# Performance work log

Measured on AMD Instinct MI355X. Metric: run time of the kernel, lower is better.

The kernel has to match this reference:

```python
import jax, jax.numpy as jnp
import numpy as np

B, L, V, E, H, C, OUT = 128, 256, 50000, 300, 128, 4, 2
D = 2 * H  # features_size == sequence_max_len (required by the conv kernel width)
FS = (2, 3, 4, 5)


def _p(key, shape, s=0.05):
    return (jax.random.normal(key, shape) * s).astype(jnp.float32)


def setup_inputs() -> dict:
    key = jax.random.key(0)
    ks = jax.random.split(key, 32)
    emb = _p(ks[0], (V, E)).at[0].set(0.0)  # padding_idx=0
    inp = {
        'utterance': jax.random.randint(ks[1], (B, L), 1, V, dtype=jnp.int32),
        'seq_lengths': jnp.full((B,), L, dtype=jnp.int32),
        'emb': emb,
        'w_ih0': _p(ks[2], (2, 3 * H, E)), 'w_hh0': _p(ks[3], (2, 3 * H, H)),
        'b_ih0': _p(ks[4], (2, 3 * H)), 'b_hh0': _p(ks[5], (2, 3 * H)),
        'w_ih1': _p(ks[6], (2, 3 * H, 2 * H)), 'w_hh1': _p(ks[7], (2, 3 * H, H)),
        'b_ih1': _p(ks[8], (2, 3 * H)), 'b_hh1': _p(ks[9], (2, 3 * H)),
        'att_w': _p(ks[10], (C, D, D)), 'att_b': _p(ks[11], (C,)),
        'att_wv2': _p(ks[12], (C, D, D)), 'att_bv': _p(ks[13], (C, D)),
        'att_wv1': _p(ks[14], (C, D)),
        'fc_w': _p(ks[15], (OUT, sum(FS))), 'fc_b': _p(ks[16], (OUT,)),
    }
    for i, fs in enumerate(FS):
        inp[f'conv_w{i}'] = _p(ks[17 + 2 * i], (fs, C, fs, L))
        inp[f'conv_b{i}'] = _p(ks[18 + 2 * i], (fs,))
    return inp


def _gru_dir(x, w_ih, w_hh, b_ih, b_hh, reverse):
    # x: (B,T,in) -> (B,T,H); PyTorch GRU cell equations, eval mode (no dropout)
    gx = jnp.einsum('bti,gi->btg', x, w_ih) + b_ih  # (B,T,3H)

    def step(h, gxt):
        gh = h @ w_hh.T + b_hh
        xr, xz, xn = jnp.split(gxt, 3, axis=-1)
        hr, hz, hn = jnp.split(gh, 3, axis=-1)
        r = jax.nn.sigmoid(xr + hr)
        z = jax.nn.sigmoid(xz + hz)
        n = jnp.tanh(xn + r * hn)
        h = (1.0 - z) * n + z * h
        return h, h

    h0 = jnp.zeros((x.shape[0], w_hh.shape[1]), x.dtype)
    _, ys = jax.lax.scan(step, h0, jnp.swapaxes(gx, 0, 1), reverse=reverse)
    return jnp.swapaxes(ys, 0, 1)


def _bigru_layer(x, w_ih, w_hh, b_ih, b_hh):
    f = _gru_dir(x, w_ih[0], w_hh[0], b_ih[0], b_hh[0], False)
    b = _gru_dir(x, w_ih[1], w_hh[1], b_ih[1], b_hh[1], True)
    return jnp.concatenate([f, b], axis=-1)


def _forward(utterance, emb, w_ih0, w_hh0, b_ih0, b_hh0, w_ih1, w_hh1, b_ih1, b_hh1,
             att_w, att_b, att_wv2, att_bv, att_wv1, conv_params, fc_w, fc_b):
    x = emb[utterance]                                   # (B,L,E)
    x = _bigru_layer(x, w_ih0, w_hh0, b_ih0, b_hh0)      # (B,L,2H)
    x = _bigru_layer(x, w_ih1, w_hh1, b_ih1, b_hh1)      # (B,L,D)
    # --- AMCNN attention, vectorized over channels c ---
    mat = jnp.einsum('bld,cde->cble', x, att_w)          # mat_l per channel (C,B,L,D)
    # M_l[b,i,j] = <inputs[b,i], mat_l[b,j]> + b_l  (the torch tile/sum written as matmul)
    M = jnp.einsum('bid,cbjd->cbij', x, mat) + att_b[:, None, None, None]
    a = jax.nn.softmax(jnp.tanh(M).sum(axis=3), axis=2)  # scalar attention (C,B,L)
    g = jax.nn.sigmoid(jnp.einsum('bld,cde->cble', x, att_wv2) + att_bv[:, None, None, :])
    aa = jax.nn.softmax(jnp.einsum('cble,ce->cbl', g, att_wv1), axis=2)  # vector attn (C,B,L)
    new = jnp.einsum('cbl,bld->cbd', aa, x)              # weighted sum, broadcast over L
    Cf = a[..., None] * x[None] + new[:, :, None, :]     # (C,B,L,D)
    Cf = jnp.transpose(Cf, (1, 0, 2, 3))                 # (B,C,L,D)
    # --- conv blocks: Conv2d(k=(fs,L)) + ReLU + MaxPool((L-fs+1,1)) + Flatten ---
    pools = []
    for w, bi in conv_params:
        y = jax.lax.conv_general_dilated(Cf, w, (1, 1), 'VALID',
                                         dimension_numbers=('NCHW', 'OIHW', 'NCHW'))
        y = jax.nn.relu(y + bi[None, :, None, None])     # (B,fs,L-fs+1,1)
        pools.append(y.max(axis=(2, 3)))                 # (B,fs)
    feats = jnp.concatenate(pools, axis=-1)              # (B,sum(FS))
    return feats @ fc_w.T + fc_b                         # (B,OUT)


def reference(utterance, seq_lengths, emb, w_ih0, w_hh0, b_ih0, b_hh0,
              w_ih1, w_hh1, b_ih1, b_hh1, att_w, att_b, att_wv2, att_bv, att_wv1,
              conv_w0, conv_b0, conv_w1, conv_b1, conv_w2, conv_b2, conv_w3, conv_b3,
              fc_w, fc_b):
    # seq_lengths are all == L, so pack/pad_packed is an identity here
    conv_params = ((conv_w0, conv_b0), (conv_w1, conv_b1), (conv_w2, conv_b2), (conv_w3, conv_b3))
    return _forward(utterance, emb, w_ih0, w_hh0, b_ih0, b_hh0, w_ih1, w_hh1, b_ih1, b_hh1,
                    att_w, att_b, att_wv2, att_bv, att_wv1, conv_params, fc_w, fc_b)
```

## Files before the change

kernel.cpp:

```cpp
#include <hip/hip_runtime.h>
#include <hip/hip_bf16.h>
#include <hip/hip_fp16.h>

#define Bn  128
#define Ln  256
#define En  300
#define Hn  128
#define Cn  4
#define Dn  256
#define G3n 384
#define BLn (Bn * Ln)

typedef __hip_bfloat16 bf16;
typedef short s16x8 __attribute__((ext_vector_type(8)));
typedef float f32x4 __attribute__((ext_vector_type(4)));
typedef _Float16 h16x2 __attribute__((ext_vector_type(2)));

__device__ __forceinline__ float ldf(const float* p) { return *p; }
__device__ __forceinline__ float ldf(const bf16* p)  { return __bfloat162float(*p); }
__device__ __forceinline__ void stf(float* p, float v) { *p = v; }
__device__ __forceinline__ void stf(bf16* p, float v)  { *p = __float2bfloat16(v); }

__device__ __forceinline__ ushort f2bf(float f) {
    bf16 h = __float2bfloat16(f);
    return *reinterpret_cast<ushort*>(&h);
}

#if __has_builtin(__builtin_amdgcn_fdot2)
__device__ __forceinline__ float dot2f(h16x2 w, h16x2 h, float c) {
    return __builtin_amdgcn_fdot2(w, h, c, false);
}
#else
__device__ __forceinline__ float dot2f(h16x2 w, h16x2 h, float c) {
    return fmaf((float)w[0], (float)h[0], fmaf((float)w[1], (float)h[1], c));
}
#endif
#define BCH(x) __builtin_bit_cast(h16x2, x)

template<class OT, bool GATHER, int SM>
__global__ __launch_bounds__(256)
void gemm_mfma(const float* __restrict__ A, const float* __restrict__ W,
               const float* __restrict__ bias, OT* __restrict__ Cout,
               const int* __restrict__ gidx, int M, int N, int K)
{
    __shared__ ushort Asm[128 * 40];
    __shared__ ushort Bsm[128 * 40];
    const int bm = blockIdx.y * 128, bn = blockIdx.x * 128;
    const int tid = threadIdx.x;
    const int lane = tid & 63, w = tid >> 6, wr = w >> 1, wc = w & 1;

    const float* arow[4];
    const float* brow[4];
#pragma unroll
    for (int u = 0; u < 4; ++u) {
        const int idx = tid + u * 256;
        const int m = idx >> 3;
        arow[u] = A + (size_t)(GATHER ? gidx[bm + m] : (bm + m)) * K;
        brow[u] = W + (size_t)(bn + m) * K;
    }

    f32x4 acc[4][4] = {};
    const int nkt = (K + 31) >> 5;
    for (int kt = 0; kt < nkt; ++kt) {
        const int k0 = kt << 5;
#pragma unroll
        for (int u = 0; u < 4; ++u) {
            const int idx = tid + u * 256;
            const int m = idx >> 3, kq = idx & 7;
            const int kb = k0 + kq * 4;
            float4 v, q;
            if (kb + 4 <= K) {
                v = *(const float4*)(arow[u] + kb);
                q = *(const float4*)(brow[u] + kb);
            } else {
                v.x = kb + 0 < K ? arow[u][kb + 0] : 0.f;
                v.y = kb + 1 < K ? arow[u][kb + 1] : 0.f;
                v.z = kb + 2 < K ? arow[u][kb + 2] : 0.f;
                v.w = kb + 3 < K ? arow[u][kb + 3] : 0.f;
                q.x = kb + 0 < K ? brow[u][kb + 0] : 0.f;
                q.y = kb + 1 < K ? brow[u][kb + 1] : 0.f;
                q.z = kb + 2 < K ? brow[u][kb + 2] : 0.f;
                q.w = kb + 3 < K ? brow[u][kb + 3] : 0.f;
            }
            *(ushort4*)&Asm[m * 40 + kq * 4] =
                make_ushort4(f2bf(v.x), f2bf(v.y), f2bf(v.z), f2bf(v.w));
            *(ushort4*)&Bsm[m * 40 + kq * 4] =
                make_ushort4(f2bf(q.x), f2bf(q.y), f2bf(q.z), f2bf(q.w));
        }
        __syncthreads();
        s16x8 af[4], bfr[4];
#pragma unroll
        for (int t = 0; t < 4; ++t) {
            af[t]  = *(const s16x8*)&Asm[(wr * 64 + t * 16 + (lane & 15)) * 40 + (lane >> 4) * 8];
            bfr[t] = *(const s16x8*)&Bsm[(wc * 64 + t * 16 + (lane & 15)) * 40 + (lane >> 4) * 8];
        }
#pragma unroll
        for (int mf = 0; mf < 4; ++mf)
#pragma unroll
            for (int nf = 0; nf < 4; ++nf)
                acc[mf][nf] = __builtin_amdgcn_mfma_f32_16x16x32_bf16(
                    af[mf], bfr[nf], acc[mf][nf], 0, 0, 0);
        __syncthreads();
    }

#pragma unroll
    for (int mf = 0; mf < 4; ++mf)
#pragma unroll
        for (int nf = 0; nf < 4; ++nf) {
            const int col = bn + wc * 64 + nf * 16 + (lane & 15);
            const float bv_ = bias ? bias[col] : 0.f;
#pragma unroll
            for (int i = 0; i < 4; ++i) {
                const int row = bm + wr * 64 + mf * 16 + (lane >> 4) * 4 + i;
                const float v = acc[mf][nf][i] + bv_;
                if (SM == 1)
                    stf(&Cout[((size_t)(row >> 8) * N + col) * 256 + (row & 255)], v);
                else
                    stf(&Cout[(size_t)row * N + col], v);
            }
        }
}

__global__ __launch_bounds__(384, 1)
void gru_scan_b128(const bf16* __restrict__ gx, const float* __restrict__ w_hh,
                   const float* __restrict__ b_hh, float* __restrict__ out)
{
    const int b = blockIdx.x, dir = blockIdx.y;
    const int r = threadIdx.x;
    __shared__ __align__(16) ushort wl[384 * 136];
    __shared__ __align__(16) h16x2 hp[64];
    __shared__ float h_sh[128];
    __shared__ float rs[128], zs[128], gxn[128], ghn[128];

    const float* wbase = w_hh + (size_t)dir * G3n * Hn;
    for (int idx = r; idx < G3n * 64; idx += 384) {
        const int row = idx >> 6, k2 = idx & 63;
        const float2 v = *(const float2*)(wbase + row * Hn + 2 * k2);
        h16x2 p; p[0] = (_Float16)v.x; p[1] = (_Float16)v.y;
        *(h16x2*)&wl[row * 136 + 2 * k2] = p;
    }
    if (r < 64) { h16x2 z; z[0] = (_Float16)0.f; z[1] = (_Float16)0.f; hp[r] = z; }
    if (r < 128) h_sh[r] = 0.f;
    const float bh = b_hh[dir * G3n + r];
    __syncthreads();

    const size_t g0 = (size_t)b * Ln * 768 + dir * G3n + r
                      + (dir ? (size_t)(Ln - 1) * 768 : 0);
    const long gstep = dir ? -768L : 768L;
    float gcur = ldf(&gx[g0]);
    float gnx  = ldf(&gx[g0 + gstep]);

    const ushort* wrow = &wl[r * 136];

    for (int s = 0; s < Ln; ++s) {
        const int t = dir ? (Ln - 1 - s) : s;
        float gn2 = 0.f;
        if (s + 2 < Ln) gn2 = ldf(&gx[g0 + (long)(s + 2) * gstep]);

        float a0 = 0.f, a1 = 0.f, a2 = 0.f, a3 = 0.f;
#pragma unroll
        for (int j = 0; j < 16; ++j) {
            const float4 wv = *(const float4*)&wrow[8 * j];
            const float4 hv = *(const float4*)&hp[4 * j];
            a0 = dot2f(BCH(wv.x), BCH(hv.x), a0);
            a1 = dot2f(BCH(wv.y), BCH(hv.y), a1);
            a2 = dot2f(BCH(wv.z), BCH(hv.z), a2);
            a3 = dot2f(BCH(wv.w), BCH(hv.w), a3);
        }
        const float acc = (a0 + a1) + (a2 + a3) + bh;

        if (r < 128)      rs[r]       = 1.f / (1.f + expf(-(gcur + acc)));
        else if (r < 256) zs[r - 128] = 1.f / (1.f + expf(-(gcur + acc)));
        else { gxn[r - 256] = gcur; ghn[r - 256] = acc; }
        __syncthreads();

        if (r < 64) {
            const int j0 = 2 * r, j1 = j0 + 1;
            const float nn0 = tanhf(gxn[j0] + rs[j0] * ghn[j0]);
            const float nn1 = tanhf(gxn[j1] + rs[j1] * ghn[j1]);
            const float h0 = (1.f - zs[j0]) * nn0 + zs[j0] * h_sh[j0];
            const float h1 = (1.f - zs[j1]) * nn1 + zs[j1] * h_sh[j1];
            h_sh[j0] = h0; h_sh[j1] = h1;
            h16x2 pr; pr[0] = (_Float16)h0; pr[1] = (_Float16)h1;
            hp[r] = pr;
            *(float2*)&out[((size_t)b * Ln + t) * Dn + dir * Hn + j0] =
                make_float2(h0, h1);
        }
        __syncthreads();
        gcur = gnx; gnx = gn2;
    }
}

__global__ __launch_bounds__(256)
void attn_score_mfma(const float* __restrict__ x, const float* __restrict__ matc,
                     const float* __restrict__ attb, int c, float* __restrict__ sout)
{
    const int it = blockIdx.x, b = blockIdx.y;
    const float* A  = x    + ((size_t)b * 256 + it * 128) * 256;
    const float* Bm = matc + (size_t)b * 65536;
    __shared__ ushort Xs[128 * 40];
    __shared__ ushort Ms[128 * 40];
    const int tid = threadIdx.x, lane = tid & 63, w = tid >> 6;
    const float bc = attb[c];
    float psum[2][4] = {};

    for (int jt = 0; jt < 2; ++jt) {
        f32x4 acc[2][8] = {};
        for (int kt = 0; kt < 8; ++kt) {
            const int k0 = kt << 5;
#pragma unroll
            for (int u = 0; u < 4; ++u) {
                const int idx = tid + u * 256;
                const int m = idx >> 3, kq = idx & 7;
                const float4 v = *(const float4*)(A + (size_t)m * 256 + k0 + kq * 4);
                const float4 q = *(const float4*)(Bm + (size_t)(jt * 128 + m) * 256 + k0 + kq * 4);
                *(ushort4*)&Xs[m * 40 + kq * 4] =
                    make_ushort4(f2bf(v.x), f2bf(v.y), f2bf(v.z), f2bf(v.w));
                *(ushort4*)&Ms[m * 40 + kq * 4] =
                    make_ushort4(f2bf(q.x), f2bf(q.y), f2bf(q.z), f2bf(q.w));
            }
            __syncthreads();
            s16x8 af[2], bfr[8];
#pragma unroll
            for (int t = 0; t < 2; ++t)
                af[t] = *(const s16x8*)&Xs[(w * 32 + t * 16 + (lane & 15)) * 40 + (lane >> 4) * 8];
#pragma unroll
            for (int t = 0; t < 8; ++t)
                bfr[t] = *(const s16x8*)&Ms[(t * 16 + (lane & 15)) * 40 + (lane >> 4) * 8];
#pragma unroll
            for (int mf = 0; mf < 2; ++mf)
#pragma unroll
                for (int nf = 0; nf < 8; ++nf)
                    acc[mf][nf] = __builtin_amdgcn_mfma_f32_16x16x32_bf16(
                        af[mf], bfr[nf], acc[mf][nf], 0, 0, 0);
            __syncthreads();
        }
#pragma unroll
        for (int mf = 0; mf < 2; ++mf)
#pragma unroll
            for (int nf = 0; nf < 8; ++nf)
#pragma unroll
                for (int i = 0; i < 4; ++i)
                    psum[mf][i] += tanhf(acc[mf][nf][i] + bc);
    }

#pragma unroll
    for (int mf = 0; mf < 2; ++mf)
#pragma unroll
        for (int i = 0; i < 4; ++i) {
            float v = psum[mf][i];
            v += __shfl_xor(v, 1); v += __shfl_xor(v, 2);
            v += __shfl_xor(v, 4); v += __shfl_xor(v, 8);
            if ((lane & 15) == 0)
                sout[b * 256 + it * 128 + w * 32 + mf * 16 + (lane >> 4) * 4 + i] = v;
        }
}

__global__ __launch_bounds__(256)
void gv_reduce(const float* __restrict__ gv, const float* __restrict__ bv,
               const float* __restrict__ wv1, float* __restrict__ al)
{
    const int row = blockIdx.x * 4 + (threadIdx.x >> 6);
    const int l = threadIdx.x & 63;
    const float4 v  = *(const float4*)(gv + (size_t)row * 256 + l * 4);
    const float4 bb = *(const float4*)(bv + l * 4);
    const float4 w  = *(const float4*)(wv1 + l * 4);
    float s = w.x / (1.f + expf(-(v.x + bb.x)))
            + w.y / (1.f + expf(-(v.y + bb.y)))
            + w.z / (1.f + expf(-(v.z + bb.z)))
            + w.w / (1.f + expf(-(v.w + bb.w)));
#pragma unroll
    for (int m = 1; m < 64; m <<= 1) s += __shfl_xor(s, m);
    if (l == 0) al[row] = s;
}

__global__ void transpose256(const float* __restrict__ src, float* __restrict__ dst)
{
    const float* s = src + (size_t)blockIdx.x * 65536;
    float* d = dst + (size_t)blockIdx.x * 65536;
    __shared__ float t[32][33];
    const int tx = threadIdx.x & 31, ty8 = threadIdx.x >> 5;
    for (int bi = 0; bi < 8; ++bi)
        for (int bj = 0; bj < 8; ++bj) {
            __syncthreads();
            for (int r = ty8; r < 32; r += 8)
                t[r][tx] = s[(size_t)(bi * 32 + r) * 256 + bj * 32 + tx];
            __syncthreads();
            for (int r = ty8; r < 32; r += 8)
                d[(size_t)(bj * 32 + r) * 256 + bi * 32 + tx] = t[tx][r];
        }
}

__global__ void softmax256(const float* __restrict__ in, float* __restrict__ out)
{
    __shared__ float red[256];
    const int row = blockIdx.x, t = threadIdx.x;
    const float v = in[(size_t)row * 256 + t];
    red[t] = v; __syncthreads();
    for (int off = 128; off; off >>= 1) {
        if (t < off) red[t] = fmaxf(red[t], red[t + off]);
        __syncthreads();
    }
    const float mx = red[0]; __syncthreads();
    const float e = expf(v - mx);
    red[t] = e; __syncthreads();
    for (int off = 128; off; off >>= 1) {
        if (t < off) red[t] += red[t + off];
        __syncthreads();
    }
    out[(size_t)row * 256 + t] = e / red[0];
}

__global__ void weighted_sum_kernel(const float* __restrict__ aa,
                                    const float* __restrict__ x,
                                    float* __restrict__ outnew)
{
    const int b = blockIdx.x, c = blockIdx.y, d = threadIdx.x;
    __shared__ float w[Ln];
    w[d] = aa[((size_t)c * Bn + b) * Ln + d];
    __syncthreads();
    float acc = 0.f;
    for (int l = 0; l < Ln; ++l)
        acc += w[l] * x[((size_t)b * Ln + l) * Dn + d];
    outnew[((size_t)c * Bn + b) * Dn + d] = acc;
}

__global__ void wpack_fill(const float* __restrict__ w0, const float* __restrict__ w1,
                           const float* __restrict__ w2, const float* __restrict__ w3,
                           float* __restrict__ wp)
{
    const int f = blockIdx.x;
    if (f < 4) {
        const int cnt[4]  = {4096, 9216, 16384, 25600};
        const int boff[4] = {0, 4096, 13312, 29696};
        const float* src = f == 0 ? w0 : f == 1 ? w1 : f == 2 ? w2 : w3;
        for (int i = threadIdx.x; i < cnt[f]; i += blockDim.x)
            wp[boff[f] + i] = src[i];
    } else {
        for (int i = threadIdx.x; i < 65536 - 55296; i += blockDim.x)
            wp[55296 + i] = 0.f;
    }
}

__global__ __launch_bounds__(256)
void nwd_kernel(const float* __restrict__ nw, const float* __restrict__ wp,
                float* __restrict__ nwd)
{
    const int b = blockIdx.x;
    __shared__ float ns[4][256];
    for (int i = threadIdx.x; i < 1024; i += 256)
        ns[i >> 8][i & 255] = nw[((size_t)((i >> 8) * Bn + b) << 8) + (i & 255)];
    __syncthreads();
    const int row = threadIdx.x;
    if (row < 216) {
        int f, base;
        if (row < 16)       { f = 0; base = 0; }
        else if (row < 52)  { f = 1; base = 16; }
        else if (row < 116) { f = 2; base = 52; }
        else                { f = 3; base = 116; }
        const int fs = f + 2, local = row - base;
        const int c = (local / fs) & 3;
        const float* wr = wp + (size_t)row * 256;
        float acc = 0.f;
        for (int k = 0; k < 256; ++k) acc += ns[c][k] * wr[k];
        nwd[b * 256 + row] = acc;
    }
}

__global__ __launch_bounds__(256)
void conv_combine(const float* __restrict__ xwT, const float* __restrict__ a,
                  const float* __restrict__ nwd, const float* __restrict__ cb,
                  float* __restrict__ pool, int fs, int base, int poff)
{
    const int b = blockIdx.x, tid = threadIdx.x;
    __shared__ float ash[4][256];
    __shared__ float basev[5];
    __shared__ float red[256];
    for (int i = tid; i < 1024; i += 256)
        ash[i >> 8][i & 255] = a[((size_t)((i >> 8) * Bn + b) << 8) + (i & 255)];
    if (tid < fs) {
        float s = cb[tid];
        for (int c = 0; c < 4; ++c)
            for (int kh = 0; kh < fs; ++kh)
                s += nwd[b * 256 + base + (tid * 4 + c) * fs + kh];
        basev[tid] = s;
    }
    __syncthreads();
    const int ni = Ln - fs + 1;
    const float* xb = xwT + ((size_t)b << 16);
    for (int o = 0; o < fs; ++o) {
        float best = 0.f;
        if (tid < ni) {
            float acc = basev[o];
            for (int c = 0; c < 4; ++c)
                for (int kh = 0; kh < fs; ++kh) {
                    const int row = base + (o * 4 + c) * fs + kh;
                    acc += ash[c][tid + kh] * xb[(row << 8) + tid + kh];
                }
            best = fmaxf(acc, 0.f);
        }
        red[tid] = best; __syncthreads();
        for (int off = 128; off; off >>= 1) {
            if (tid < off) red[tid] = fmaxf(red[tid], red[tid + off]);
            __syncthreads();
        }
        if (tid == 0) pool[b * 14 + poff + o] = red[0];
        __syncthreads();
    }
}

__global__ void fc_kernel(const float* __restrict__ pool, const float* __restrict__ fw,
                          const float* __restrict__ fb, float* __restrict__ out)
{
    const int i = threadIdx.x;
    const int b = i >> 1, o = i & 1;
    float acc = fb[o];
#pragma unroll
    for (int f = 0; f < 14; ++f) acc += pool[b * 14 + f] * fw[o * 14 + f];
    out[i] = acc;
}

extern "C" void kernel_launch(void* const* d_in, const int* in_sizes, int n_in,
                              void* d_out, int out_size, void* d_ws, size_t ws_size,
                              hipStream_t stream)
{
    const int*   utt    = (const int*)  d_in[0];
    const float* emb    = (const float*)d_in[2];
    const float* w_ih0  = (const float*)d_in[3];
    const float* w_hh0  = (const float*)d_in[4];
    const float* b_ih0  = (const float*)d_in[5];
    const float* b_hh0  = (const float*)d_in[6];
    const float* w_ih1  = (const float*)d_in[7];
    const float* w_hh1  = (const float*)d_in[8];
    const float* b_ih1  = (const float*)d_in[9];
    const float* b_hh1  = (const float*)d_in[10];
    const float* att_w  = (const float*)d_in[11];
    const float* att_b  = (const float*)d_in[12];
    const float* att_wv2= (const float*)d_in[13];
    const float* att_bv = (const float*)d_in[14];
    const float* att_wv1= (const float*)d_in[15];
    const float* fc_w   = (const float*)d_in[16];
    const float* fc_b   = (const float*)d_in[17];
    const float* cw[4] = {(const float*)d_in[18], (const float*)d_in[20],
                          (const float*)d_in[22], (const float*)d_in[24]};
    const float* cb[4] = {(const float*)d_in[19], (const float*)d_in[21],
                          (const float*)d_in[23], (const float*)d_in[25]};

    float* ws = (float*)d_ws;
    bf16*  GX   = (bf16*)ws;
    float* H1   = ws + 12582912;
    float* H2   = H1 + 8388608;
    float* WT   = H2 + 8388608;
    float* WP   = WT + 262144;
    float* S    = WP + 65536;
    float* Aa   = S + 131072;
    float* AL   = Aa + 131072;
    float* AAa  = AL + 131072;
    float* NEW_ = AAa + 131072;
    float* NWD  = NEW_ + 131072;
    float* POOL = NWD + 32768;
    float* MATc = H1;
    float* GV   = ws;
    float* XWT  = ws;

    gemm_mfma<bf16, true, 0><<<dim3(6, 256), 256, 0, stream>>>(
        emb, w_ih0, b_ih0, GX, utt, BLn, 768, En);
    gru_scan_b128<<<dim3(Bn, 2), 384, 0, stream>>>(GX, w_hh0, b_hh0, H1);
    gemm_mfma<bf16, false, 0><<<dim3(6, 256), 256, 0, stream>>>(
        H1, w_ih1, b_ih1, GX, nullptr, BLn, 768, Dn);
    gru_scan_b128<<<dim3(Bn, 2), 384, 0, stream>>>(GX, w_hh1, b_hh1, H2);

    transpose256<<<4, 256, 0, stream>>>(att_w, WT);
    for (int c = 0; c < 4; ++c) {
        gemm_mfma<float, false, 0><<<dim3(2, 256), 256, 0, stream>>>(
            H2, WT + (size_t)c * 65536, nullptr, MATc, nullptr, BLn, Dn, Dn);
        attn_score_mfma<<<dim3(2, Bn), 256, 0, stream>>>(
            H2, MATc, att_b, c, S + (size_t)c * 32768);
    }
    softmax256<<<Cn * Bn, 256, 0, stream>>>(S, Aa);

    transpose256<<<4, 256, 0, stream>>>(att_wv2, WT);
    for (int c = 0; c < 4; ++c) {
        gemm_mfma<float, false, 0><<<dim3(2, 256), 256, 0, stream>>>(
            H2, WT + (size_t)c * 65536, nullptr, GV, nullptr, BLn, Dn, Dn);
        gv_reduce<<<BLn / 4, 256, 0, stream>>>(
            GV, att_bv + c * Dn, att_wv1 + c * Dn, AL + (size_t)c * BLn);
    }
    softmax256<<<Cn * Bn, 256, 0, stream>>>(AL, AAa);
    weighted_sum_kernel<<<dim3(Bn, Cn), 256, 0, stream>>>(AAa, H2, NEW_);

    wpack_fill<<<5, 256, 0, stream>>>(cw[0], cw[1], cw[2], cw[3], WP);
    gemm_mfma<float, false, 1><<<dim3(2, 256), 256, 0, stream>>>(
        H2, WP, nullptr, XWT, nullptr, BLn, Dn, Dn);
    nwd_kernel<<<Bn, 256, 0, stream>>>(NEW_, WP, NWD);

    const int baserow[4] = {0, 16, 52, 116};
    const int poff[4]    = {0, 2, 5, 9};
    for (int f = 0; f < 4; ++f)
        conv_combine<<<Bn, 256, 0, stream>>>(XWT, Aa, NWD, cb[f], POOL, f + 2, baserow[f], poff[f]);

    fc_kernel<<<1, 256, 0, stream>>>(POOL, fc_w, fc_b, (float*)d_out);
}
```

Before: 1.290 ms.

## Store GRU hidden states and attention intermediates in bf16; broadcast h via readlane

Hidden-state buffers H1/H2, the transposed attention weights, and the intermediate MATc/GV products are now stored in bf16 rather than fp32. The GEMM is templated on input types so these can be loaded directly, roughly halving global memory traffic in the attention and conv GEMMs. The GRU scan now has 128 threads perform the update, one element each. The recurrent matvec loads each lane's slice of h once and broadcasts it across the wave with readlane instead of re-reading shared memory per iteration. This trades some accuracy from bf16 storage for reduced bandwidth and fewer LDS reads on the serial critical path.

```diff
diff --git a/kernel.cpp b/kernel.cpp
--- a/kernel.cpp
+++ b/kernel.cpp
@@ -25,6 +25,10 @@
     bf16 h = __float2bfloat16(f);
     return *reinterpret_cast<ushort*>(&h);
 }
+__device__ __forceinline__ float bfu(ushort x) {
+    unsigned t = ((unsigned)x) << 16;
+    return __builtin_bit_cast(float, t);
+}
 
 #if __has_builtin(__builtin_amdgcn_fdot2)
 __device__ __forceinline__ float dot2f(h16x2 w, h16x2 h, float c) {
@@ -37,9 +41,20 @@
 #endif
 #define BCH(x) __builtin_bit_cast(h16x2, x)
 
-template<class OT, bool GATHER, int SM>
+__device__ __forceinline__ float rdl(float v, int l) {
+    return __builtin_bit_cast(float,
+        __builtin_amdgcn_readlane(__builtin_bit_cast(int, v), l));
+}
+
+__device__ __forceinline__ float4 ld4f(const float* p) { return *(const float4*)p; }
+__device__ __forceinline__ float4 ld4f(const bf16* p) {
+    ushort4 u = *(const ushort4*)p;
+    return make_float4(bfu(u.x), bfu(u.y), bfu(u.z), bfu(u.w));
+}
+
+template<class AT, class WTp, class OT, bool GATHER, int SM>
 __global__ __launch_bounds__(256)
-void gemm_mfma(const float* __restrict__ A, const float* __restrict__ W,
+void gemm_mfma(const AT* __restrict__ A, const WTp* __restrict__ W,
                const float* __restrict__ bias, OT* __restrict__ Cout,
                const int* __restrict__ gidx, int M, int N, int K)
 {
@@ -49,8 +64,8 @@
     const int tid = threadIdx.x;
     const int lane = tid & 63, w = tid >> 6, wr = w >> 1, wc = w & 1;
 
-    const float* arow[4];
-    const float* brow[4];
+    const AT* arow[4];
+    const WTp* brow[4];
 #pragma unroll
     for (int u = 0; u < 4; ++u) {
         const int idx = tid + u * 256;
@@ -70,17 +85,17 @@
             const int kb = k0 + kq * 4;
             float4 v, q;
             if (kb + 4 <= K) {
-                v = *(const float4*)(arow[u] + kb);
-                q = *(const float4*)(brow[u] + kb);
+                v = ld4f(arow[u] + kb);
+                q = ld4f(brow[u] + kb);
             } else {
-                v.x = kb + 0 < K ? arow[u][kb + 0] : 0.f;
-                v.y = kb + 1 < K ? arow[u][kb + 1] : 0.f;
-                v.z = kb + 2 < K ? arow[u][kb + 2] : 0.f;
-                v.w = kb + 3 < K ? arow[u][kb + 3] : 0.f;
-                q.x = kb + 0 < K ? brow[u][kb + 0] : 0.f;
-                q.y = kb + 1 < K ? brow[u][kb + 1] : 0.f;
-                q.z = kb + 2 < K ? brow[u][kb + 2] : 0.f;
-                q.w = kb + 3 < K ? brow[u][kb + 3] : 0.f;
+                v.x = kb + 0 < K ? ldf(&arow[u][kb + 0]) : 0.f;
+                v.y = kb + 1 < K ? ldf(&arow[u][kb + 1]) : 0.f;
+                v.z = kb + 2 < K ? ldf(&arow[u][kb + 2]) : 0.f;
+                v.w = kb + 3 < K ? ldf(&arow[u][kb + 3]) : 0.f;
+                q.x = kb + 0 < K ? ldf(&brow[u][kb + 0]) : 0.f;
+                q.y = kb + 1 < K ? ldf(&brow[u][kb + 1]) : 0.f;
+                q.z = kb + 2 < K ? ldf(&brow[u][kb + 2]) : 0.f;
+                q.w = kb + 3 < K ? ldf(&brow[u][kb + 3]) : 0.f;
             }
             *(ushort4*)&Asm[m * 40 + kq * 4] =
                 make_ushort4(f2bf(v.x), f2bf(v.y), f2bf(v.z), f2bf(v.w));
@@ -122,13 +137,14 @@
 }
 
 __global__ __launch_bounds__(384, 1)
-void gru_scan_b128(const bf16* __restrict__ gx, const float* __restrict__ w_hh,
-                   const float* __restrict__ b_hh, float* __restrict__ out)
+void gru_scan_v8(const bf16* __restrict__ gx, const float* __restrict__ w_hh,
+                 const float* __restrict__ b_hh, bf16* __restrict__ out)
 {
     const int b = blockIdx.x, dir = blockIdx.y;
     const int r = threadIdx.x;
+    const int lane = r & 63;
     __shared__ __align__(16) ushort wl[384 * 136];
-    __shared__ __align__(16) h16x2 hp[64];
+    __shared__ __align__(16) ushort hp16[128];
     __shared__ float h_sh[128];
     __shared__ float rs[128], zs[128], gxn[128], ghn[128];
 
@@ -139,8 +155,7 @@
         h16x2 p; p[0] = (_Float16)v.x; p[1] = (_Float16)v.y;
         *(h16x2*)&wl[row * 136 + 2 * k2] = p;
     }
-    if (r < 64) { h16x2 z; z[0] = (_Float16)0.f; z[1] = (_Float16)0.f; hp[r] = z; }
-    if (r < 128) h_sh[r] = 0.f;
+    if (r < 128) { hp16[r] = 0; h_sh[r] = 0.f; }
     const float bh = b_hh[dir * G3n + r];
     __syncthreads();
 
@@ -157,15 +172,16 @@
         float gn2 = 0.f;
         if (s + 2 < Ln) gn2 = ldf(&gx[g0 + (long)(s + 2) * gstep]);
 
+        const float4 hown = *(const float4*)&hp16[(lane & 15) * 8];
+
         float a0 = 0.f, a1 = 0.f, a2 = 0.f, a3 = 0.f;
 #pragma unroll
         for (int j = 0; j < 16; ++j) {
             const float4 wv = *(const float4*)&wrow[8 * j];
-            const float4 hv = *(const float4*)&hp[4 * j];
-            a0 = dot2f(BCH(wv.x), BCH(hv.x), a0);
-            a1 = dot2f(BCH(wv.y), BCH(hv.y), a1);
-            a2 = dot2f(BCH(wv.z), BCH(hv.z), a2);
-            a3 = dot2f(BCH(wv.w), BCH(hv.w), a3);
+            a0 = dot2f(BCH(wv.x), BCH(rdl(hown.x, j)), a0);
+            a1 = dot2f(BCH(wv.y), BCH(rdl(hown.y, j)), a1);
+            a2 = dot2f(BCH(wv.z), BCH(rdl(hown.z, j)), a2);
+            a3 = dot2f(BCH(wv.w), BCH(rdl(hown.w, j)), a3);
         }
         const float acc = (a0 + a1) + (a2 + a3) + bh;
 
@@ -174,17 +190,14 @@
         else { gxn[r - 256] = gcur; ghn[r - 256] = acc; }
         __syncthreads();
 
-        if (r < 64) {
-            const int j0 = 2 * r, j1 = j0 + 1;
-            const float nn0 = tanhf(gxn[j0] + rs[j0] * ghn[j0]);
-            const float nn1 = tanhf(gxn[j1] + rs[j1] * ghn[j1]);
-            const float h0 = (1.f - zs[j0]) * nn0 + zs[j0] * h_sh[j0];
-            const float h1 = (1.f - zs[j1]) * nn1 + zs[j1] * h_sh[j1];
-            h_sh[j0] = h0; h_sh[j1] = h1;
-            h16x2 pr; pr[0] = (_Float16)h0; pr[1] = (_Float16)h1;
-            hp[r] = pr;
-            *(float2*)&out[((size_t)b * Ln + t) * Dn + dir * Hn + j0] =
-                make_float2(h0, h1);
+        if (r < 128) {
+            const int j = r;
+            const float nn = tanhf(gxn[j] + rs[j] * ghn[j]);
+            const float hnew = (1.f - zs[j]) * nn + zs[j] * h_sh[j];
+            h_sh[j] = hnew;
+            const _Float16 hf = (_Float16)hnew;
+            hp16[j] = __builtin_bit_cast(ushort, hf);
+            out[((size_t)b * Ln + t) * Dn + dir * Hn + j] = __float2bfloat16(hnew);
         }
         __syncthreads();
         gcur = gnx; gnx = gn2;
@@ -192,12 +205,12 @@
 }
 
 __global__ __launch_bounds__(256)
-void attn_score_mfma(const float* __restrict__ x, const float* __restrict__ matc,
+void attn_score_mfma(const bf16* __restrict__ x, const bf16* __restrict__ matc,
                      const float* __restrict__ attb, int c, float* __restrict__ sout)
 {
     const int it = blockIdx.x, b = blockIdx.y;
-    const float* A  = x    + ((size_t)b * 256 + it * 128) * 256;
-    const float* Bm = matc + (size_t)b * 65536;
+    const bf16* A  = x    + ((size_t)b * 256 + it * 128) * 256;
+    const bf16* Bm = matc + (size_t)b * 65536;
     __shared__ ushort Xs[128 * 40];
     __shared__ ushort Ms[128 * 40];
     const int tid = threadIdx.x, lane = tid & 63, w = tid >> 6;
@@ -209,15 +222,13 @@
         for (int kt = 0; kt < 8; ++kt) {
             const int k0 = kt << 5;
 #pragma unroll
-            for (int u = 0; u < 4; ++u) {
+            for (int u = 0; u < 2; ++u) {
                 const int idx = tid + u * 256;
-                const int m = idx >> 3, kq = idx & 7;
-                const float4 v = *(const float4*)(A + (size_t)m * 256 + k0 + kq * 4);
-                const float4 q = *(const float4*)(Bm + (size_t)(jt * 128 + m) * 256 + k0 + kq * 4);
-                *(ushort4*)&Xs[m * 40 + kq * 4] =
-                    make_ushort4(f2bf(v.x), f2bf(v.y), f2bf(v.z), f2bf(v.w));
-                *(ushort4*)&Ms[m * 40 + kq * 4] =
-                    make_ushort4(f2bf(q.x), f2bf(q.y), f2bf(q.z), f2bf(q.w));
+                const int m = idx >> 2, q = idx & 3;
+                *(s16x8*)&Xs[m * 40 + q * 8] =
+                    *(const s16x8*)&A[(size_t)m * 256 + k0 + q * 8];
+                *(s16x8*)&Ms[m * 40 + q * 8] =
+                    *(const s16x8*)&Bm[(size_t)(jt * 128 + m) * 256 + k0 + q * 8];
             }
             __syncthreads();
             s16x8 af[2], bfr[8];
@@ -257,27 +268,27 @@
 }
 
 __global__ __launch_bounds__(256)
-void gv_reduce(const float* __restrict__ gv, const float* __restrict__ bv,
+void gv_reduce(const bf16* __restrict__ gv, const float* __restrict__ bv,
                const float* __restrict__ wv1, float* __restrict__ al)
 {
     const int row = blockIdx.x * 4 + (threadIdx.x >> 6);
     const int l = threadIdx.x & 63;
-    const float4 v  = *(const float4*)(gv + (size_t)row * 256 + l * 4);
+    const ushort4 u = *(const ushort4*)&gv[(size_t)row * 256 + l * 4];
     const float4 bb = *(const float4*)(bv + l * 4);
     const float4 w  = *(const float4*)(wv1 + l * 4);
-    float s = w.x / (1.f + expf(-(v.x + bb.x)))
-            + w.y / (1.f + expf(-(v.y + bb.y)))
-            + w.z / (1.f + expf(-(v.z + bb.z)))
-            + w.w / (1.f + expf(-(v.w + bb.w)));
+    float s = w.x / (1.f + expf(-(bfu(u.x) + bb.x)))
+            + w.y / (1.f + expf(-(bfu(u.y) + bb.y)))
+            + w.z / (1.f + expf(-(bfu(u.z) + bb.z)))
+            + w.w / (1.f + expf(-(bfu(u.w) + bb.w)));
 #pragma unroll
     for (int m = 1; m < 64; m <<= 1) s += __shfl_xor(s, m);
     if (l == 0) al[row] = s;
 }
 
-__global__ void transpose256(const float* __restrict__ src, float* __restrict__ dst)
+__global__ void transpose256(const float* __restrict__ src, bf16* __restrict__ dst)
 {
     const float* s = src + (size_t)blockIdx.x * 65536;
-    float* d = dst + (size_t)blockIdx.x * 65536;
+    bf16* d = dst + (size_t)blockIdx.x * 65536;
     __shared__ float t[32][33];
     const int tx = threadIdx.x & 31, ty8 = threadIdx.x >> 5;
     for (int bi = 0; bi < 8; ++bi)
@@ -287,7 +298,7 @@
                 t[r][tx] = s[(size_t)(bi * 32 + r) * 256 + bj * 32 + tx];
             __syncthreads();
             for (int r = ty8; r < 32; r += 8)
-                d[(size_t)(bj * 32 + r) * 256 + bi * 32 + tx] = t[tx][r];
+                stf(&d[(size_t)(bj * 32 + r) * 256 + bi * 32 + tx], t[tx][r]);
         }
 }
 
@@ -312,7 +323,7 @@
 }
 
 __global__ void weighted_sum_kernel(const float* __restrict__ aa,
-                                    const float* __restrict__ x,
+                                    const bf16* __restrict__ x,
                                     float* __restrict__ outnew)
 {
     const int b = blockIdx.x, c = blockIdx.y, d = threadIdx.x;
@@ -321,7 +332,7 @@
     __syncthreads();
     float acc = 0.f;
     for (int l = 0; l < Ln; ++l)
-        acc += w[l] * x[((size_t)b * Ln + l) * Dn + d];
+        acc += w[l] * ldf(&x[((size_t)b * Ln + l) * Dn + d]);
     outnew[((size_t)c * Bn + b) * Dn + d] = acc;
 }
 
@@ -448,10 +459,10 @@
 
     float* ws = (float*)d_ws;
     bf16*  GX   = (bf16*)ws;
-    float* H1   = ws + 12582912;
-    float* H2   = H1 + 8388608;
-    float* WT   = H2 + 8388608;
-    float* WP   = WT + 262144;
+    bf16*  H1   = (bf16*)(ws + 12582912);
+    bf16*  H2   = (bf16*)(ws + 12582912 + 4194304);
+    bf16*  WT   = (bf16*)(ws + 20971520);
+    float* WP   = ws + 20971520 + 131072;
     float* S    = WP + 65536;
     float* Aa   = S + 131072;
     float* AL   = Aa + 131072;
@@ -459,20 +470,20 @@
     float* NEW_ = AAa + 131072;
     float* NWD  = NEW_ + 131072;
     float* POOL = NWD + 32768;
-    float* MATc = H1;
-    float* GV   = ws;
+    bf16*  MATc = H1;
+    bf16*  GV   = (bf16*)ws;
     float* XWT  = ws;
 
-    gemm_mfma<bf16, true, 0><<<dim3(6, 256), 256, 0, stream>>>(
+    gemm_mfma<float, float, bf16, true, 0><<<dim3(6, 256), 256, 0, stream>>>(
         emb, w_ih0, b_ih0, GX, utt, BLn, 768, En);
-    gru_scan_b128<<<dim3(Bn, 2), 384, 0, stream>>>(GX, w_hh0, b_hh0, H1);
-    gemm_mfma<bf16, false, 0><<<dim3(6, 256), 256, 0, stream>>>(
+    gru_scan_v8<<<dim3(Bn, 2), 384, 0, stream>>>(GX, w_hh0, b_hh0, H1);
+    gemm_mfma<bf16, float, bf16, false, 0><<<dim3(6, 256), 256, 0, stream>>>(
         H1, w_ih1, b_ih1, GX, nullptr, BLn, 768, Dn);
-    gru_scan_b128<<<dim3(Bn, 2), 384, 0, stream>>>(GX, w_hh1, b_hh1, H2);
+    gru_scan_v8<<<dim3(Bn, 2), 384, 0, stream>>>(GX, w_hh1, b_hh1, H2);
 
     transpose256<<<4, 256, 0, stream>>>(att_w, WT);
     for (int c = 0; c < 4; ++c) {
-        gemm_mfma<float, false, 0><<<dim3(2, 256), 256, 0, stream>>>(
+        gemm_mfma<bf16, bf16, bf16, false, 0><<<dim3(2, 256), 256, 0, stream>>>(
             H2, WT + (size_t)c * 65536, nullptr, MATc, nullptr, BLn, Dn, Dn);
         attn_score_mfma<<<dim3(2, Bn), 256, 0, stream>>>(
             H2, MATc, att_b, c, S + (size_t)c * 32768);
@@ -481,7 +492,7 @@
 
     transpose256<<<4, 256, 0, stream>>>(att_wv2, WT);
     for (int c = 0; c < 4; ++c) {
-        gemm_mfma<float, false, 0><<<dim3(2, 256), 256, 0, stream>>>(
+        gemm_mfma<bf16, bf16, bf16, false, 0><<<dim3(2, 256), 256, 0, stream>>>(
             H2, WT + (size_t)c * 65536, nullptr, GV, nullptr, BLn, Dn, Dn);
         gv_reduce<<<BLn / 4, 256, 0, stream>>>(
             GV, att_bv + c * Dn, att_wv1 + c * Dn, AL + (size_t)c * BLn);
@@ -490,7 +501,7 @@
     weighted_sum_kernel<<<dim3(Bn, Cn), 256, 0, stream>>>(AAa, H2, NEW_);
 
     wpack_fill<<<5, 256, 0, stream>>>(cw[0], cw[1], cw[2], cw[3], WP);
-    gemm_mfma<float, false, 1><<<dim3(2, 256), 256, 0, stream>>>(
+    gemm_mfma<bf16, float, float, false, 1><<<dim3(2, 256), 256, 0, stream>>>(
         H2, WP, nullptr, XWT, nullptr, BLn, Dn, Dn);
     nwd_kernel<<<Bn, 256, 0, stream>>>(NEW_, WP, NWD);
 
```

Result: no change. 1.291 ms (+0.1%).
